# Kernel optimization log

Measured on AMD Instinct MI355X. Metric: run time of the kernel, lower is better.

The kernel has to match this reference:

```python
import jax, jax.numpy as jnp
from jax import lax
import numpy as np

C, C_MID, K_ENC, K_UP, SCALE = 128, 64, 3, 5, 2
B, H, W = 4, 48, 48
BN_EPS = 1e-3  # ultralytics Conv BN eps
EPS = 1e-6


def setup_inputs() -> dict:
    key = jax.random.key(0)
    ks = jax.random.split(key, 12)
    n_enc = (SCALE * K_UP) ** 2  # 100
    return {
        "x": jax.random.uniform(ks[0], (B, C, H, W), dtype=jnp.float32),
        "comp_w": jax.random.normal(ks[1], (C_MID, C, 1, 1), dtype=jnp.float32) * 0.05,
        "comp_bn_g": jax.random.normal(ks[2], (C_MID,), dtype=jnp.float32) * 0.1 + 1.0,
        "comp_bn_b": jax.random.normal(ks[3], (C_MID,), dtype=jnp.float32) * 0.1,
        "comp_bn_m": jax.random.normal(ks[4], (C_MID,), dtype=jnp.float32) * 0.1,
        "comp_bn_v": jax.random.uniform(ks[5], (C_MID,), dtype=jnp.float32, minval=0.5, maxval=1.5),
        "enc_w": jax.random.normal(ks[6], (n_enc, C_MID, K_ENC, K_ENC), dtype=jnp.float32) * 0.05,
        "enc_bn_g": jax.random.normal(ks[7], (n_enc,), dtype=jnp.float32) * 0.1 + 1.0,
        "enc_bn_b": jax.random.normal(ks[8], (n_enc,), dtype=jnp.float32) * 0.1,
        "enc_bn_m": jax.random.normal(ks[9], (n_enc,), dtype=jnp.float32) * 0.1,
        "enc_bn_v": jax.random.uniform(ks[10], (n_enc,), dtype=jnp.float32, minval=0.5, maxval=1.5),
    }


def _conv_bn(x, w, g, b, m, v, pad, act):
    y = lax.conv_general_dilated(
        x, w, window_strides=(1, 1), padding=[(pad, pad), (pad, pad)],
        dimension_numbers=("NCHW", "OIHW", "NCHW"))
    scale = (g * lax.rsqrt(v + BN_EPS))[None, :, None, None]
    y = (y - m[None, :, None, None]) * scale + b[None, :, None, None]
    if act:  # SiLU
        y = y * jax.nn.sigmoid(y)
    return y


def reference(x, comp_w, comp_bn_g, comp_bn_b, comp_bn_m, comp_bn_v,
              enc_w, enc_bn_g, enc_bn_b, enc_bn_m, enc_bn_v):
    b, c, h, w = x.shape
    h_, w_ = h * SCALE, w * SCALE

    # ---- SAGamma: self-adaptive gamma correction ----
    gray = 0.299 * x[:, 0] + 0.587 * x[:, 1] + 0.114 * x[:, 2]  # (b,h,w)
    gm = jnp.mean(gray, axis=(1, 2), keepdims=True)              # (b,1,1)
    gs = jnp.std(gray, axis=(1, 2), ddof=1, keepdims=True)       # unbiased, like torch
    gamma = 0.8 + (1.2 - 0.8) * gm / (gm + jnp.maximum(gs, EPS))
    gamma = jnp.clip(gamma, 0.8, 1.2)[:, None]                   # (b,1,1,1)
    x = jnp.power(x + EPS, gamma)

    # ---- CARAFE ----
    # kernel prediction: comp (1x1 Conv+BN+SiLU) -> enc (3x3 Conv+BN, no act)
    Wk = _conv_bn(x, comp_w, comp_bn_g, comp_bn_b, comp_bn_m, comp_bn_v, pad=0, act=True)
    Wk = _conv_bn(Wk, enc_w, enc_bn_g, enc_bn_b, enc_bn_m, enc_bn_v, pad=K_ENC // 2, act=False)
    # pixel shuffle: (b, 25*s*s, h, w) -> (b, 25, h_, w_)
    k2 = K_UP * K_UP
    Wk = Wk.reshape(b, k2, SCALE, SCALE, h, w)
    Wk = Wk.transpose(0, 1, 4, 2, 5, 3).reshape(b, k2, h_, w_)
    Wk = jax.nn.softmax(Wk, axis=1)

    # nearest upsample x2
    Xu = jnp.repeat(jnp.repeat(x, SCALE, axis=2), SCALE, axis=3)  # (b,c,h_,w_)
    # unfold with kernel 5, dilation 2, pad 4 -> (b,c,25,h_,w_), torch (c,kh,kw) ordering
    pad = (K_UP // 2) * SCALE
    Xp = jnp.pad(Xu, ((0, 0), (0, 0), (pad, pad), (pad, pad)))
    patches = jnp.stack(
        [Xp[:, :, i * SCALE:i * SCALE + h_, j * SCALE:j * SCALE + w_]
         for i in range(K_UP) for j in range(K_UP)], axis=2)      # (b,c,25,h_,w_)

    return jnp.einsum("bkhw,bckhw->bchw", Wk, patches)
```

## Files before the change

kernel.cpp:

```cpp
#include <hip/hip_runtime.h>
#include <hip/hip_bf16.h>
#include <math.h>

#define CB   128
#define CMID 64
#define NENC 100
#define HH   48
#define WW   48
#define BB   4
#define HW   (HH*WW)
#define H2   (HH*2)
#define W2   (WW*2)
#define PS   56
#define PROWS 50
#define PCOL0 4
#define PLANE (PROWS*PS)
#define EG   2

__global__ void halo_kernel(float* __restrict__ y1p) {
    int idx = blockIdx.x * blockDim.x + threadIdx.x;
    int plane = idx / 124;
    int t = idx % 124;
    float* p = y1p + (size_t)plane * PLANE;
    float4 z = make_float4(0.f, 0.f, 0.f, 0.f);
    if (t < 14) {
        *(float4*)(p + t * 4) = z;
    } else if (t < 28) {
        *(float4*)(p + 49 * PS + (t - 14) * 4) = z;
    } else {
        int s = t - 28;
        int r = 1 + (s >> 1);
        int col = (s & 1) ? 52 : 0;
        *(float4*)(p + r * PS + col) = z;
    }
}

__global__ void gamma_kernel(const float* __restrict__ x, float* __restrict__ gamma) {
    int b = blockIdx.x;
    const float* xb = x + (size_t)b * CB * HW;
    const float4* R4 = (const float4*)xb;
    const float4* G4 = (const float4*)(xb + HW);
    const float4* B4 = (const float4*)(xb + 2 * HW);
    float s = 0.f, s2 = 0.f;
    for (int i = threadIdx.x; i < HW / 4; i += blockDim.x) {
        float4 r = R4[i], g = G4[i], bl = B4[i];
        float g0 = 0.299f * r.x + 0.587f * g.x + 0.114f * bl.x;
        float g1 = 0.299f * r.y + 0.587f * g.y + 0.114f * bl.y;
        float g2 = 0.299f * r.z + 0.587f * g.z + 0.114f * bl.z;
        float g3 = 0.299f * r.w + 0.587f * g.w + 0.114f * bl.w;
        s  += (g0 + g1) + (g2 + g3);
        s2 += (g0 * g0 + g1 * g1) + (g2 * g2 + g3 * g3);
    }
    for (int o = 32; o > 0; o >>= 1) {
        s  += __shfl_down(s, o);
        s2 += __shfl_down(s2, o);
    }
    __shared__ float ss[4], ss2[4];
    int wid = threadIdx.x >> 6;
    if ((threadIdx.x & 63) == 0) { ss[wid] = s; ss2[wid] = s2; }
    __syncthreads();
    if (threadIdx.x == 0) {
        float S = 0.f, S2 = 0.f;
        int nw = blockDim.x >> 6;
        for (int i = 0; i < nw; i++) { S += ss[i]; S2 += ss2[i]; }
        const float N = (float)HW;
        float gm = S / N;
        float var = (S2 - S * S / N) / (N - 1.0f);
        var = fmaxf(var, 0.f);
        float gs = sqrtf(var);
        float gam = 0.8f + 0.4f * gm / (gm + fmaxf(gs, 1e-6f));
        gam = fminf(fmaxf(gam, 0.8f), 1.2f);
        gamma[b] = gam;
    }
}

__global__ void pow_kernel(const float* __restrict__ x, const float* __restrict__ gamma,
                           float* __restrict__ xg) {
    int idx = blockIdx.x * blockDim.x + threadIdx.x;
    const int total4 = BB * CB * HW / 4;
    if (idx >= total4) return;
    int b = idx / (CB * HW / 4);
    float gam = gamma[b];
    float4 xv = ((const float4*)x)[idx];
    float4 r;
    r.x = __expf(gam * __logf(xv.x + 1e-6f));
    r.y = __expf(gam * __logf(xv.y + 1e-6f));
    r.z = __expf(gam * __logf(xv.z + 1e-6f));
    r.w = __expf(gam * __logf(xv.w + 1e-6f));
    ((float4*)xg)[idx] = r;
}

__global__ void conv1_kernel(const float* __restrict__ xg, const float* __restrict__ w,
                             const float* __restrict__ g, const float* __restrict__ bta,
                             const float* __restrict__ m, const float* __restrict__ vv,
                             float* __restrict__ y1p) {
    int idx = blockIdx.x * blockDim.x + threadIdx.x;
    const int PG = HW / 4;
    const int total = BB * CMID * PG;
    if (idx >= total) return;
    int pg = idx % PG;
    int cm = (idx / PG) % CMID;
    int b  = idx / (CMID * PG);
    const float4* xb = (const float4*)(xg + (size_t)b * CB * HW) + pg;
    const float* wc = w + cm * CB;
    float4 acc = {0.f, 0.f, 0.f, 0.f};
#pragma unroll 8
    for (int c = 0; c < CB; c++) {
        float4 xv = xb[(size_t)c * PG];
        float wv = wc[c];
        acc.x = fmaf(wv, xv.x, acc.x);
        acc.y = fmaf(wv, xv.y, acc.y);
        acc.z = fmaf(wv, xv.z, acc.z);
        acc.w = fmaf(wv, xv.w, acc.w);
    }
    float sc = g[cm] * rsqrtf(vv[cm] + 1e-3f);
    float sh = bta[cm] - m[cm] * sc;
    float4 o;
    float t;
    t = acc.x * sc + sh; o.x = t / (1.f + __expf(-t));
    t = acc.y * sc + sh; o.y = t / (1.f + __expf(-t));
    t = acc.z * sc + sh; o.z = t / (1.f + __expf(-t));
    t = acc.w * sc + sh; o.w = t / (1.f + __expf(-t));
    int row = pg / 12, col = (pg % 12) * 4;
    float* dst = y1p + ((size_t)(b * CMID + cm)) * PLANE + (row + 1) * PS + (col + PCOL0);
    *(float4*)dst = o;
}

#define FMA4(A0,A1,A2,A3, wa,wb,wc, lf,mm,rt) \
    A0 = fmaf(wa, lf,   fmaf(wb, mm.x, fmaf(wc, mm.y, A0))); \
    A1 = fmaf(wa, mm.x, fmaf(wb, mm.y, fmaf(wc, mm.z, A1))); \
    A2 = fmaf(wa, mm.y, fmaf(wb, mm.z, fmaf(wc, mm.w, A2))); \
    A3 = fmaf(wa, mm.z, fmaf(wb, mm.w, fmaf(wc, rt,   A3)));

__global__ __launch_bounds__(192) void conv3_kernel(
        const float* __restrict__ y1p, const float* __restrict__ w,
        const float* __restrict__ g, const float* __restrict__ bta,
        const float* __restrict__ m, const float* __restrict__ vv,
        float* __restrict__ wk2n) {
    int blk = blockIdx.x;
    int eg  = blk % (NENC / EG);
    int tmp = blk / (NENC / EG);
    int rb  = tmp % 3, b = tmp / 3;
    int e0  = eg * EG;
    int t   = threadIdx.x;
    int row = rb * 16 + t / 12;
    int c0  = (t % 12) * 4;
    const float* wb0 = w + (size_t)e0 * CMID * 9;
    const float* wb1 = wb0 + CMID * 9;
    const float* yb = y1p + (size_t)b * CMID * PLANE + row * PS + (c0 + PCOL0);

    float a00 = 0.f, a01 = 0.f, a02 = 0.f, a03 = 0.f;
    float a10 = 0.f, a11 = 0.f, a12 = 0.f, a13 = 0.f;

    float  lf0 = yb[-1];        float4 m0 = *(const float4*)yb;          float rt0 = yb[4];
    float  lf1 = yb[PS-1];      float4 m1 = *(const float4*)(yb+PS);     float rt1 = yb[PS+4];
    float  lf2 = yb[2*PS-1];    float4 m2 = *(const float4*)(yb+2*PS);   float rt2 = yb[2*PS+4];
    float u00 = wb0[0], u01 = wb0[1], u02 = wb0[2];
    float u10 = wb0[3], u11 = wb0[4], u12 = wb0[5];
    float u20 = wb0[6], u21 = wb0[7], u22 = wb0[8];
    float v00 = wb1[0], v01 = wb1[1], v02 = wb1[2];
    float v10 = wb1[3], v11 = wb1[4], v12 = wb1[5];
    float v20 = wb1[6], v21 = wb1[7], v22 = wb1[8];

    for (int cm = 0; cm < CMID - 1; ++cm) {
        const float* yn = yb + (size_t)(cm + 1) * PLANE;
        float  nlf0 = yn[-1];       float4 nm0 = *(const float4*)yn;         float nrt0 = yn[4];
        float  nlf1 = yn[PS-1];     float4 nm1 = *(const float4*)(yn+PS);    float nrt1 = yn[PS+4];
        float  nlf2 = yn[2*PS-1];   float4 nm2 = *(const float4*)(yn+2*PS);  float nrt2 = yn[2*PS+4];
        const float* wn0 = wb0 + (cm + 1) * 9;
        const float* wn1 = wb1 + (cm + 1) * 9;
        float nu00 = wn0[0], nu01 = wn0[1], nu02 = wn0[2];
        float nu10 = wn0[3], nu11 = wn0[4], nu12 = wn0[5];
        float nu20 = wn0[6], nu21 = wn0[7], nu22 = wn0[8];
        float nv00 = wn1[0], nv01 = wn1[1], nv02 = wn1[2];
        float nv10 = wn1[3], nv11 = wn1[4], nv12 = wn1[5];
        float nv20 = wn1[6], nv21 = wn1[7], nv22 = wn1[8];

        FMA4(a00,a01,a02,a03, u00,u01,u02, lf0,m0,rt0)
        FMA4(a00,a01,a02,a03, u10,u11,u12, lf1,m1,rt1)
        FMA4(a00,a01,a02,a03, u20,u21,u22, lf2,m2,rt2)
        FMA4(a10,a11,a12,a13, v00,v01,v02, lf0,m0,rt0)
        FMA4(a10,a11,a12,a13, v10,v11,v12, lf1,m1,rt1)
        FMA4(a10,a11,a12,a13, v20,v21,v22, lf2,m2,rt2)

        lf0 = nlf0; m0 = nm0; rt0 = nrt0;
        lf1 = nlf1; m1 = nm1; rt1 = nrt1;
        lf2 = nlf2; m2 = nm2; rt2 = nrt2;
        u00 = nu00; u01 = nu01; u02 = nu02;
        u10 = nu10; u11 = nu11; u12 = nu12;
        u20 = nu20; u21 = nu21; u22 = nu22;
        v00 = nv00; v01 = nv01; v02 = nv02;
        v10 = nv10; v11 = nv11; v12 = nv12;
        v20 = nv20; v21 = nv21; v22 = nv22;
    }
    FMA4(a00,a01,a02,a03, u00,u01,u02, lf0,m0,rt0)
    FMA4(a00,a01,a02,a03, u10,u11,u12, lf1,m1,rt1)
    FMA4(a00,a01,a02,a03, u20,u21,u22, lf2,m2,rt2)
    FMA4(a10,a11,a12,a13, v00,v01,v02, lf0,m0,rt0)
    FMA4(a10,a11,a12,a13, v10,v11,v12, lf1,m1,rt1)
    FMA4(a10,a11,a12,a13, v20,v21,v22, lf2,m2,rt2)

    float sc0 = g[e0] * rsqrtf(vv[e0] + 1e-3f);
    float sh0 = bta[e0] - m[e0] * sc0;
    float sc1 = g[e0+1] * rsqrtf(vv[e0+1] + 1e-3f);
    float sh1 = bta[e0+1] - m[e0+1] * sc1;
    int kk = e0 >> 2, off0 = e0 & 3;
    float* op = wk2n + (((size_t)(b * 25 + kk) * HW + row * WW + c0) << 2) + off0;
    *(float2*)(op + 0)  = make_float2(a00*sc0+sh0, a10*sc1+sh1);
    *(float2*)(op + 4)  = make_float2(a01*sc0+sh0, a11*sc1+sh1);
    *(float2*)(op + 8)  = make_float2(a02*sc0+sh0, a12*sc1+sh1);
    *(float2*)(op + 12) = make_float2(a03*sc0+sh0, a13*sc1+sh1);
}

__global__ __launch_bounds__(256) void sg_kernel(const float* __restrict__ xg,
                                                 const float* __restrict__ wk2n,
                                                 float* __restrict__ out) {
    int blk = blockIdx.x;
    int whalf = blk & 1;
    int bh = blk >> 1;
    int h = bh % HH, b = bh / HH;
    int tid = threadIdx.x;

    __shared__ float raw[25 * 24 * 4];
    __shared__ float wsm[25 * 2 * 48];

    {
        const float4* w4p = (const float4*)wk2n;
        size_t base4 = (size_t)b * 25 * HW + h * WW + whalf * 24;
        float4* raw4 = (float4*)raw;
        for (int t = tid; t < 600; t += 256) {
            int k = t / 24, wl = t % 24;
            raw4[t] = w4p[base4 + (size_t)k * HW + wl];
        }
    }
    __syncthreads();
    if (tid < 96) {
        int wl = tid >> 2, off = tid & 3;
        float v[25]; float mx = -1e30f;
#pragma unroll
        for (int k = 0; k < 25; k++) { v[k] = raw[(k * 24 + wl) * 4 + off]; mx = fmaxf(mx, v[k]); }
        float sum = 0.f;
#pragma unroll
        for (int k = 0; k < 25; k++) { v[k] = __expf(v[k] - mx); sum += v[k]; }
        float inv = 1.f / sum;
        int si = off >> 1, sj = off & 1;
#pragma unroll
        for (int k = 0; k < 25; k++) wsm[k * 96 + si * 48 + 2 * wl + sj] = v[k] * inv;
    }
    __syncthreads();

    int c = tid >> 1, q = tid & 1;
    const float* xb = xg + ((size_t)b * CB + c) * HW;
    int wbase = whalf * 24 + q * 12;
    float* ob = out + (((size_t)b * CB + c) * H2 + 2 * h) * W2;
    const float4* wsm4 = (const float4*)wsm;
    const float4 Z4 = make_float4(0.f, 0.f, 0.f, 0.f);

    float4 A[5], Bv[5], Cv[5];
#pragma unroll
    for (int i = 0; i < 5; i++) {
        int hr = h + i - 2;
        bool rv = (hr >= 0) && (hr < HH);
        const float* rp = xb + hr * WW;
        A[i]  = (rv && wbase > 0) ? *(const float4*)(rp + wbase - 4) : Z4;
        Bv[i] = rv                ? *(const float4*)(rp + wbase)     : Z4;
        Cv[i] = rv                ? *(const float4*)(rp + wbase + 4) : Z4;
    }

#pragma unroll
    for (int s = 0; s < 3; s++) {
        int wc = wbase + 4 * s;
        float acc0[8], acc1[8];
#pragma unroll
        for (int p = 0; p < 8; p++) { acc0[p] = 0.f; acc1[p] = 0.f; }
#pragma unroll
        for (int i = 0; i < 5; i++) {
            float xv[12] = {A[i].x, A[i].y, A[i].z, A[i].w,
                            Bv[i].x, Bv[i].y, Bv[i].z, Bv[i].w,
                            Cv[i].x, Cv[i].y, Cv[i].z, Cv[i].w};
#pragma unroll
            for (int j = 0; j < 5; j++) {
                int k = i * 5 + j;
                float4 w0a = wsm4[k * 24 + 6 * q + 2 * s];
                float4 w0b = wsm4[k * 24 + 6 * q + 2 * s + 1];
                float4 w1a = wsm4[k * 24 + 12 + 6 * q + 2 * s];
                float4 w1b = wsm4[k * 24 + 12 + 6 * q + 2 * s + 1];
                float x0 = xv[j + 2], x1 = xv[j + 3], x2 = xv[j + 4], x3 = xv[j + 5];
                acc0[0] = fmaf(w0a.x, x0, acc0[0]); acc0[1] = fmaf(w0a.y, x0, acc0[1]);
                acc0[2] = fmaf(w0a.z, x1, acc0[2]); acc0[3] = fmaf(w0a.w, x1, acc0[3]);
                acc0[4] = fmaf(w0b.x, x2, acc0[4]); acc0[5] = fmaf(w0b.y, x2, acc0[5]);
                acc0[6] = fmaf(w0b.z, x3, acc0[6]); acc0[7] = fmaf(w0b.w, x3, acc0[7]);
                acc1[0] = fmaf(w1a.x, x0, acc1[0]); acc1[1] = fmaf(w1a.y, x0, acc1[1]);
                acc1[2] = fmaf(w1a.z, x1, acc1[2]); acc1[3] = fmaf(w1a.w, x1, acc1[3]);
                acc1[4] = fmaf(w1b.x, x2, acc1[4]); acc1[5] = fmaf(w1b.y, x2, acc1[5]);
                acc1[6] = fmaf(w1b.z, x3, acc1[6]); acc1[7] = fmaf(w1b.w, x3, acc1[7]);
            }
        }
        int colg = whalf * 48 + 24 * q + 8 * s;
        *(float4*)(ob + colg)          = make_float4(acc0[0], acc0[1], acc0[2], acc0[3]);
        *(float4*)(ob + colg + 4)      = make_float4(acc0[4], acc0[5], acc0[6], acc0[7]);
        *(float4*)(ob + W2 + colg)     = make_float4(acc1[0], acc1[1], acc1[2], acc1[3]);
        *(float4*)(ob + W2 + colg + 4) = make_float4(acc1[4], acc1[5], acc1[6], acc1[7]);
        if (s < 2) {
            int nc = wc + 8;
#pragma unroll
            for (int i = 0; i < 5; i++) {
                int hr = h + i - 2;
                bool rv = (hr >= 0) && (hr < HH);
                A[i] = Bv[i]; Bv[i] = Cv[i];
                Cv[i] = (rv && nc < WW) ? *(const float4*)(xb + hr * WW + nc) : Z4;
            }
        }
    }
}

extern "C" void kernel_launch(void* const* d_in, const int* in_sizes, int n_in,
                              void* d_out, int out_size, void* d_ws, size_t ws_size,
                              hipStream_t stream) {
    const float* x       = (const float*)d_in[0];
    const float* comp_w  = (const float*)d_in[1];
    const float* comp_g  = (const float*)d_in[2];
    const float* comp_b  = (const float*)d_in[3];
    const float* comp_m  = (const float*)d_in[4];
    const float* comp_v  = (const float*)d_in[5];
    const float* enc_w   = (const float*)d_in[6];
    const float* enc_g   = (const float*)d_in[7];
    const float* enc_b   = (const float*)d_in[8];
    const float* enc_m   = (const float*)d_in[9];
    const float* enc_v   = (const float*)d_in[10];
    float* out = (float*)d_out;

    float* ws = (float*)d_ws;
    float* gamma = ws;
    float* xg    = ws + 64;
    float* wk2n  = xg + (size_t)BB * CB * HW;
    float* y1p   = wk2n + (size_t)BB * 25 * HW * 4;

    halo_kernel<<<(BB * CMID * 124) / 256, 256, 0, stream>>>(y1p);
    gamma_kernel<<<BB, 256, 0, stream>>>(x, gamma);
    {
        int total4 = BB * CB * HW / 4;
        pow_kernel<<<(total4 + 255) / 256, 256, 0, stream>>>(x, gamma, xg);
    }
    {
        int total = BB * CMID * (HW / 4);
        conv1_kernel<<<(total + 255) / 256, 256, 0, stream>>>(
            xg, comp_w, comp_g, comp_b, comp_m, comp_v, y1p);
    }
    conv3_kernel<<<BB * 3 * (NENC / EG), 192, 0, stream>>>(
        y1p, enc_w, enc_g, enc_b, enc_m, enc_v, wk2n);
    sg_kernel<<<BB * HH * 2, 256, 0, stream>>>(xg, wk2n, out);
}
```

Baseline: 168.1 us.

## Fuse halo zeroing and gamma reduction into the pow kernel

Removes the separate halo-zeroing and gamma-statistics kernels. Each pow block now recomputes the per-batch gray mean and std over the first three channels itself, then applies the power and zeroes its share of the conv1 padding halo. This cuts two launches and the serial 4-block gamma kernel. In exchange every block redundantly reads the three input channels (HW*3 floats), which adds L2 traffic.

Result: faster. 163.3 us (-2.9%).

```diff
diff --git a/kernel.cpp b/kernel.cpp
--- a/kernel.cpp
+++ b/kernel.cpp
@@ -16,33 +16,21 @@
 #define PCOL0 4
 #define PLANE (PROWS*PS)
 #define EG   2
-
-__global__ void halo_kernel(float* __restrict__ y1p) {
-    int idx = blockIdx.x * blockDim.x + threadIdx.x;
-    int plane = idx / 124;
-    int t = idx % 124;
-    float* p = y1p + (size_t)plane * PLANE;
-    float4 z = make_float4(0.f, 0.f, 0.f, 0.f);
-    if (t < 14) {
-        *(float4*)(p + t * 4) = z;
-    } else if (t < 28) {
-        *(float4*)(p + 49 * PS + (t - 14) * 4) = z;
-    } else {
-        int s = t - 28;
-        int r = 1 + (s >> 1);
-        int col = (s & 1) ? 52 : 0;
-        *(float4*)(p + r * PS + col) = z;
-    }
-}
-
-__global__ void gamma_kernel(const float* __restrict__ x, float* __restrict__ gamma) {
-    int b = blockIdx.x;
+#define NHALO4 (BB*CMID*124)
+
+__global__ __launch_bounds__(256) void pow_kernel(const float* __restrict__ x,
+                                                  float* __restrict__ xg,
+                                                  float* __restrict__ y1p) {
+    int tid = threadIdx.x;
+    int bid = blockIdx.x;
+    int b = bid / (CB * HW / 4 / 256);
+
     const float* xb = x + (size_t)b * CB * HW;
     const float4* R4 = (const float4*)xb;
     const float4* G4 = (const float4*)(xb + HW);
     const float4* B4 = (const float4*)(xb + 2 * HW);
     float s = 0.f, s2 = 0.f;
-    for (int i = threadIdx.x; i < HW / 4; i += blockDim.x) {
+    for (int i = tid; i < HW / 4; i += 256) {
         float4 r = R4[i], g = G4[i], bl = B4[i];
         float g0 = 0.299f * r.x + 0.587f * g.x + 0.114f * bl.x;
         float g1 = 0.299f * r.y + 0.587f * g.y + 0.114f * bl.y;
@@ -55,32 +43,25 @@
         s  += __shfl_down(s, o);
         s2 += __shfl_down(s2, o);
     }
-    __shared__ float ss[4], ss2[4];
-    int wid = threadIdx.x >> 6;
-    if ((threadIdx.x & 63) == 0) { ss[wid] = s; ss2[wid] = s2; }
+    __shared__ float ss[4], ss2[4], gsh;
+    int wid = tid >> 6;
+    if ((tid & 63) == 0) { ss[wid] = s; ss2[wid] = s2; }
     __syncthreads();
-    if (threadIdx.x == 0) {
-        float S = 0.f, S2 = 0.f;
-        int nw = blockDim.x >> 6;
-        for (int i = 0; i < nw; i++) { S += ss[i]; S2 += ss2[i]; }
+    if (tid == 0) {
+        float S = ss[0] + ss[1] + ss[2] + ss[3];
+        float S2 = ss2[0] + ss2[1] + ss2[2] + ss2[3];
         const float N = (float)HW;
         float gm = S / N;
         float var = (S2 - S * S / N) / (N - 1.0f);
         var = fmaxf(var, 0.f);
         float gs = sqrtf(var);
         float gam = 0.8f + 0.4f * gm / (gm + fmaxf(gs, 1e-6f));
-        gam = fminf(fmaxf(gam, 0.8f), 1.2f);
-        gamma[b] = gam;
-    }
-}
-
-__global__ void pow_kernel(const float* __restrict__ x, const float* __restrict__ gamma,
-                           float* __restrict__ xg) {
-    int idx = blockIdx.x * blockDim.x + threadIdx.x;
-    const int total4 = BB * CB * HW / 4;
-    if (idx >= total4) return;
-    int b = idx / (CB * HW / 4);
-    float gam = gamma[b];
+        gsh = fminf(fmaxf(gam, 0.8f), 1.2f);
+    }
+    __syncthreads();
+    float gam = gsh;
+
+    int idx = bid * 256 + tid;
     float4 xv = ((const float4*)x)[idx];
     float4 r;
     r.x = __expf(gam * __logf(xv.x + 1e-6f));
@@ -88,6 +69,23 @@
     r.z = __expf(gam * __logf(xv.z + 1e-6f));
     r.w = __expf(gam * __logf(xv.w + 1e-6f));
     ((float4*)xg)[idx] = r;
+
+    if (idx < NHALO4) {
+        int plane = idx / 124;
+        int t = idx % 124;
+        float* p = y1p + (size_t)plane * PLANE;
+        float4 z = make_float4(0.f, 0.f, 0.f, 0.f);
+        if (t < 14) {
+            *(float4*)(p + t * 4) = z;
+        } else if (t < 28) {
+            *(float4*)(p + 49 * PS + (t - 14) * 4) = z;
+        } else {
+            int sIdx = t - 28;
+            int rr = 1 + (sIdx >> 1);
+            int col = (sIdx & 1) ? 52 : 0;
+            *(float4*)(p + rr * PS + col) = z;
+        }
+    }
 }
 
 __global__ void conv1_kernel(const float* __restrict__ xg, const float* __restrict__ w,
@@ -331,16 +329,13 @@
     float* out = (float*)d_out;
 
     float* ws = (float*)d_ws;
-    float* gamma = ws;
-    float* xg    = ws + 64;
+    float* xg    = ws;
     float* wk2n  = xg + (size_t)BB * CB * HW;
     float* y1p   = wk2n + (size_t)BB * 25 * HW * 4;
 
-    halo_kernel<<<(BB * CMID * 124) / 256, 256, 0, stream>>>(y1p);
-    gamma_kernel<<<BB, 256, 0, stream>>>(x, gamma);
     {
         int total4 = BB * CB * HW / 4;
-        pow_kernel<<<(total4 + 255) / 256, 256, 0, stream>>>(x, gamma, xg);
+        pow_kernel<<<total4 / 256, 256, 0, stream>>>(x, xg, y1p);
     }
     {
         int total = BB * CMID * (HW / 4);
```
